# Optimization experiments

Hardware: AMD Instinct MI355X
Metric: run time of the kernel (lower is better)

## Reference

```python
import jax, jax.numpy as jnp
import numpy as np

HEADS, HEAD_DIM, WS = 12, 32, 7
DISP = WS // 2


def _shift_masks(ws, d):
    # upper/lower mask: blocks crossing the wrapped boundary in the row direction
    ul = np.zeros((ws * ws, ws * ws), np.float32)
    ul[-d * ws:, :-d * ws] = -np.inf
    ul[:-d * ws, -d * ws:] = -np.inf
    # left/right mask: columns crossing the wrapped boundary
    lr = np.zeros((ws, ws, ws, ws), np.float32)
    lr[:, -d:, :, :-d] = -np.inf
    lr[:, :-d, :, -d:] = -np.inf
    lr = lr.reshape(ws * ws, ws * ws)
    return jnp.asarray(ul), jnp.asarray(lr)


def _rel_indices(ws):
    idx = np.arange(ws)
    coords = np.stack(np.meshgrid(idx, idx, indexing='ij'), -1).reshape(-1, 2)  # [[x,y] row-major]
    rel = coords[None, :, :] - coords[:, None, :] + ws - 1  # (ws^2, ws^2, 2)
    return jnp.asarray(rel)


def setup_inputs() -> dict:
    key = jax.random.key(0)
    ks = jax.random.split(key, 7)
    b, H, W, dim = 16, 56, 56, 384
    inner = HEADS * HEAD_DIM
    x = jax.random.normal(ks[0], (b, H, W, dim), jnp.float32)
    w_qkv = jax.random.normal(ks[1], (dim, 3 * inner), jnp.float32) * (dim ** -0.5)
    pos_embedding = jax.random.normal(ks[2], (2 * WS - 1, 2 * WS - 1), jnp.float32) * 0.02
    w_out = jax.random.normal(ks[3], (inner, dim), jnp.float32) * (inner ** -0.5)
    b_out = jnp.zeros((dim,), jnp.float32)
    w_post = jax.random.normal(ks[4], (dim, dim), jnp.float32) * (dim ** -0.5)
    b_post = jnp.zeros((dim,), jnp.float32)
    return {"x": x, "w_qkv": w_qkv, "pos_embedding": pos_embedding,
            "w_out": w_out, "b_out": b_out, "w_post": w_post, "b_post": b_post}


def reference(x, w_qkv, pos_embedding, w_out, b_out, w_post, b_post):
    b, H, W, dim = x.shape
    nw_h, nw_w = H // WS, W // WS
    scale = HEAD_DIM ** -0.5

    # cyclic shift
    x = jnp.roll(x, shift=(-DISP, -DISP), axis=(1, 2))

    # qkv projection (no bias), window partition -> (3, b, h, nw, ws^2, d)
    qkv = (x @ w_qkv).reshape(b, nw_h, WS, nw_w, WS, 3, HEADS, HEAD_DIM)
    qkv = qkv.transpose(5, 0, 6, 1, 3, 2, 4, 7).reshape(3, b, HEADS, nw_h * nw_w, WS * WS, HEAD_DIM)
    q, k, v = qkv[0], qkv[1], qkv[2]

    dots = jnp.einsum('bhwid,bhwjd->bhwij', q, k) * scale

    # relative position bias gather
    rel = _rel_indices(WS)
    dots = dots + pos_embedding[rel[..., 0], rel[..., 1]]

    # shifted-window masks
    ul, lr = _shift_masks(WS, DISP)
    dots = dots.at[:, :, -nw_w:].add(ul)
    dots = dots.at[:, :, nw_w - 1::nw_w].add(lr)

    attn = jax.nn.softmax(dots, axis=-1)
    out = jnp.einsum('bhwij,bhwjd->bhwid', attn, v)

    # merge windows back -> (b, H, W, inner)
    out = out.reshape(b, HEADS, nw_h, nw_w, WS, WS, HEAD_DIM)
    out = out.transpose(0, 2, 4, 3, 5, 1, 6).reshape(b, H, W, HEADS * HEAD_DIM)

    out = out @ w_out + b_out
    out = out @ w_post + b_post  # post_drop is identity in eval
    out = jnp.roll(out, shift=(DISP, DISP), axis=(1, 2))
    return out
```

## Files before the change

### kernel.cpp

```cpp
#include <hip/hip_runtime.h>
#include <hip/hip_bf16.h>
#include <stdint.h>

typedef __bf16 bf16_t;
typedef bf16_t bf16x8 __attribute__((ext_vector_type(8)));
typedef bf16_t bf16x4 __attribute__((ext_vector_type(4)));
typedef float f32x4 __attribute__((ext_vector_type(4)));

#define BATCH 16
#define HH    56
#define DIMK  384
#define M_TOT (BATCH*HH*HH)
#define SCALE 0.17677669529663687f

__device__ __forceinline__ void async_load16(const bf16_t* g, const bf16_t* l) {
  __builtin_amdgcn_global_load_lds((const __attribute__((address_space(1))) void*)g,
                                   (__attribute__((address_space(3))) void*)l,
                                   16, 0, 0);
}

template<int CTRL>
__device__ __forceinline__ float dpp_ror(float x) {
  return __int_as_float(__builtin_amdgcn_mov_dpp(__float_as_int(x), CTRL, 0xf, 0xf, false));
}
__device__ __forceinline__ float rowmax16(float v) {
  v = fmaxf(v, dpp_ror<0x121>(v));
  v = fmaxf(v, dpp_ror<0x122>(v));
  v = fmaxf(v, dpp_ror<0x124>(v));
  v = fmaxf(v, dpp_ror<0x128>(v));
  return v;
}
__device__ __forceinline__ float rowsum16(float v) {
  v += dpp_ror<0x121>(v);
  v += dpp_ror<0x122>(v);
  v += dpp_ror<0x124>(v);
  v += dpp_ror<0x128>(v);
  return v;
}

__global__ void k_zero(float* __restrict__ p, int n) {
  int i = blockIdx.x * 256 + threadIdx.x;
  if (i < n) p[i] = 0.f;
}

__global__ void k_transpose(const float* __restrict__ w, bf16_t* __restrict__ wT) {
  int idx = blockIdx.x * 256 + threadIdx.x;
  if (idx >= 1152 * 384) return;
  int n = idx / 384, k = idx - n * 384;
  wT[idx] = (bf16_t)w[k * 1152 + n];
}

__global__ void k_comb(const float* __restrict__ w_out, const float* __restrict__ b_out,
                       const float* __restrict__ w_post, const float* __restrict__ b_post,
                       bf16_t* __restrict__ wcombT, float* __restrict__ bcomb) {
  __shared__ float col[384];
  const int n = blockIdx.x, t = threadIdx.x;
  for (int j = t; j < 384; j += 256) col[j] = w_post[j * 384 + n];
  __syncthreads();
  for (int k = t; k < 384; k += 256) {
    float acc = 0.f;
    for (int j = 0; j < 384; ++j) acc += w_out[k * 384 + j] * col[j];
    wcombT[n * 384 + k] = (bf16_t)acc;
  }
  if (t == 0) {
    float acc = b_post[n];
    for (int j = 0; j < 384; ++j) acc += b_out[j] * col[j];
    bcomb[n] = acc;
  }
}

__global__ void k_bias(const float* __restrict__ pos, float* __restrict__ biasC) {
  int idx = blockIdx.x * 256 + threadIdx.x;
  if (idx >= 4 * 16 * 64 * 4) return;
  int reg = idx & 3, lane = (idx >> 2) & 63, tile = (idx >> 8) & 15, cls = idx >> 12;
  int mt = tile >> 2, nt = tile & 3, lc = lane & 15, quad = lane >> 4;
  int m = mt * 16 + quad * 4 + reg, n = nt * 16 + lc;
  float v = -1e32f;
  if (m < 49 && n < 49) {
    int ty = m / 7, tx = m % 7, jy = n / 7, jx = n % 7;
    bool dead = ((cls & 1) && ((m >= 28) != (n >= 28))) ||
                ((cls & 2) && ((tx >= 4) != (jx >= 4)));
    v = dead ? -1e32f : pos[(jy - ty + 6) * 13 + (jx - tx + 6)] * (1.0f / SCALE);
  }
  biasC[idx] = v;
}

__global__ void k_convroll(const float* __restrict__ x, bf16_t* __restrict__ xb) {
  int idx = blockIdx.x * 256 + threadIdx.x;
  if (idx >= M_TOT * 48) return;
  int row = idx / 48, c = idx - row * 48;
  int bb = row / 3136, rem = row - bb * 3136, i = rem / 56, j = rem - i * 56;
  int si = i + 3; if (si >= 56) si -= 56;
  int sj = j + 3; if (sj >= 56) sj -= 56;
  const float* src = x + ((size_t)(bb * 3136 + si * 56 + sj)) * 384 + c * 8;
  f32x4 v0 = *(const f32x4*)src;
  f32x4 v1 = *(const f32x4*)(src + 4);
  bf16x8 o;
#pragma unroll
  for (int u = 0; u < 4; ++u) { o[u] = (bf16_t)v0[u]; o[4 + u] = (bf16_t)v1[u]; }
  *(bf16x8*)(xb + (size_t)row * 384 + c * 8) = o;
}

template<int MODE>
__device__ __forceinline__
void gemm_body(const bf16_t* __restrict__ A, const bf16_t* __restrict__ B,
               void* __restrict__ Cv, const float* __restrict__ bias,
               int Ndim, int Kdim, int lda) {
  __shared__ __align__(16) bf16_t As[2][128 * 64];
  __shared__ __align__(16) bf16_t Bs[2][128 * 64];
  const int tid  = threadIdx.x;
  const int wave = tid >> 6;
  const int lane = tid & 63;
  const int wr = wave >> 1, wc = wave & 1;

  const int gx   = gridDim.x;
  const int nwg  = gx * gridDim.y;
  const int flat = blockIdx.y * gx + blockIdx.x;
  const int qch  = nwg >> 3;
  const int nf   = (flat & 7) * qch + (flat >> 3);
  const int bx   = nf % gx;
  const int by   = nf / gx;

  const int row0 = by * 128;
  const int col0 = bx * 128;

  const bf16_t* aptr[4];
  const bf16_t* bptr[4];
  int dst[4];
#pragma unroll
  for (int c = 0; c < 4; ++c) {
    int linear = c * 256 + tid;
    int r  = linear >> 3;
    int kc = linear & 7;
    int gk = kc ^ (r & 7);
    dst[c] = linear * 8;
    aptr[c] = A + (size_t)(row0 + r) * lda + gk * 8;
    bptr[c] = B + (size_t)(col0 + r) * Kdim + gk * 8;
  }

  f32x4 acc[4][4] = {};
  const int lr = lane >> 4;
  const int lc = lane & 15;
  unsigned aoff[4][2], boff[4][2];
#pragma unroll
  for (int mi = 0; mi < 4; ++mi)
#pragma unroll
    for (int kh = 0; kh < 2; ++kh) {
      int arow = wr * 64 + mi * 16 + lc;
      int brow = wc * 64 + mi * 16 + lc;
      int sc   = (kh * 4 + lr) ^ (lc & 7);
      aoff[mi][kh] = (unsigned)(arow * 64 + sc * 8);
      boff[mi][kh] = (unsigned)(brow * 64 + sc * 8);
    }

  const int kiters = Kdim >> 6;

#pragma unroll
  for (int c = 0; c < 4; ++c) {
    async_load16(aptr[c], As[0] + dst[c]);
    async_load16(bptr[c], Bs[0] + dst[c]);
  }

  for (int kt = 0; kt < kiters; ++kt) {
    const int cur = kt & 1;
    __syncthreads();
    if (kt + 1 < kiters) {
      const int koff = (kt + 1) * 64;
#pragma unroll
      for (int c = 0; c < 4; ++c) {
        async_load16(aptr[c] + koff, As[cur ^ 1] + dst[c]);
        async_load16(bptr[c] + koff, Bs[cur ^ 1] + dst[c]);
      }
    }
    bf16x8 af[4][2], bfr[4][2];
#pragma unroll
    for (int mi = 0; mi < 4; ++mi)
#pragma unroll
      for (int kh = 0; kh < 2; ++kh) {
        af[mi][kh]  = *(const bf16x8*)(As[cur] + aoff[mi][kh]);
        bfr[mi][kh] = *(const bf16x8*)(Bs[cur] + boff[mi][kh]);
      }
#pragma unroll
    for (int kh = 0; kh < 2; ++kh)
#pragma unroll
      for (int mi = 0; mi < 4; ++mi)
#pragma unroll
        for (int ni = 0; ni < 4; ++ni)
          acc[mi][ni] = __builtin_amdgcn_mfma_f32_16x16x32_bf16(af[mi][kh], bfr[ni][kh], acc[mi][ni], 0, 0, 0);
  }

#pragma unroll
  for (int mi = 0; mi < 4; ++mi) {
#pragma unroll
    for (int rr = 0; rr < 4; ++rr) {
      int grow = row0 + wr * 64 + mi * 16 + lr * 4 + rr;
      size_t orow;
      if (MODE == 1) {
        int bb  = grow / 3136;
        int rem = grow - bb * 3136;
        int i = rem / 56;
        int j = rem - i * 56;
        int si = i + 3; if (si >= 56) si -= 56;
        int sj = j + 3; if (sj >= 56) sj -= 56;
        orow = (size_t)(bb * 3136 + si * 56 + sj);
      } else {
        orow = (size_t)grow;
      }
#pragma unroll
      for (int ni = 0; ni < 4; ++ni) {
        int gcol = col0 + wc * 64 + ni * 16 + lc;
        float v = acc[mi][ni][rr];
        if (MODE == 1) {
          ((float*)Cv)[orow * (size_t)Ndim + gcol] = v + bias[gcol];
        } else {
          ((bf16_t*)Cv)[orow * (size_t)Ndim + gcol] = (bf16_t)v;
        }
      }
    }
  }
}

__global__ __launch_bounds__(256)
void k_gemm_qkv(const bf16_t* __restrict__ A, const bf16_t* __restrict__ B,
                void* __restrict__ Cv, const float* __restrict__ bias,
                int Ndim, int Kdim, int lda) {
  gemm_body<0>(A, B, Cv, bias, Ndim, Kdim, lda);
}
__global__ __launch_bounds__(256)
void k_gemm_out(const bf16_t* __restrict__ A, const bf16_t* __restrict__ B,
                void* __restrict__ Cv, const float* __restrict__ bias,
                int Ndim, int Kdim, int lda) {
  gemm_body<1>(A, B, Cv, bias, Ndim, Kdim, lda);
}

__global__ __launch_bounds__(256)
void k_attn(const float* __restrict__ biasC, bf16_t* __restrict__ qkv) {
  __shared__ __align__(16) bf16_t Ps[4 * 64 * 72];
  const int tid = threadIdx.x, wid = tid >> 6, lane = tid & 63;
  const int p = blockIdx.x * 4 + wid;
  const int b = p / 768, rem = p - b * 768;
  const int head = rem >> 6, w = rem & 63;
  const int wy = w >> 3, wx = w & 7;
  const int cls = ((wy == 7) ? 1 : 0) | ((wx == 7) ? 2 : 0);
  const int lc = lane & 15, quad = lane >> 4;
  const size_t wbase = ((size_t)b * 3136 + (size_t)wy * 7 * 56 + (size_t)wx * 7) * 1152
                       + head * 32;

  auto rowoff = [&](int m) -> size_t {
    int ty = m / 7, tx = m - ty * 7;
    return wbase + (size_t)(ty * 56 + tx) * 1152;
  };

  bf16x8 qf[4], kf[4];
#pragma unroll
  for (int t = 0; t < 4; ++t) {
    int m = t * 16 + lc; if (m > 48) m = 48;
    const bf16_t* r = qkv + rowoff(m);
    qf[t] = *(const bf16x8*)(r + quad * 8);
    kf[t] = *(const bf16x8*)(r + 384 + quad * 8);
  }

  bf16x8 vf[2][2];
#pragma unroll
  for (int kc = 0; kc < 2; ++kc)
#pragma unroll
    for (int u = 0; u < 8; ++u) {
      int n = kc * 32 + quad * 8 + u; if (n > 48) n = 48;
      const bf16_t* r = qkv + rowoff(n) + 768 + lc;
      vf[kc][0][u] = r[0];
      vf[kc][1][u] = r[16];
    }

  f32x4 acc[4][4];
  const float* bp = biasC + cls * 4096 + lane * 4;
#pragma unroll
  for (int mt = 0; mt < 4; ++mt)
#pragma unroll
    for (int nt = 0; nt < 4; ++nt)
      acc[mt][nt] = *(const f32x4*)(bp + (mt * 4 + nt) * 256);
  __builtin_amdgcn_s_setprio(1);
#pragma unroll
  for (int mt = 0; mt < 4; ++mt)
#pragma unroll
    for (int nt = 0; nt < 4; ++nt)
      acc[mt][nt] = __builtin_amdgcn_mfma_f32_16x16x32_bf16(qf[mt], kf[nt], acc[mt][nt], 0, 0, 0);
  __builtin_amdgcn_s_setprio(0);

  float l[4][4];
#pragma unroll
  for (int mt = 0; mt < 4; ++mt)
#pragma unroll
    for (int reg = 0; reg < 4; ++reg) {
      float mx = fmaxf(fmaxf(acc[mt][0][reg], acc[mt][1][reg]),
                       fmaxf(acc[mt][2][reg], acc[mt][3][reg]));
      mx = rowmax16(mx);
      float s = 0.f;
#pragma unroll
      for (int nt = 0; nt < 4; ++nt) {
        float pe = __expf((acc[mt][nt][reg] - mx) * SCALE);
        acc[mt][nt][reg] = pe;
        s += pe;
      }
      l[mt][reg] = rowsum16(s);
    }

  bf16_t* P = Ps + wid * (64 * 72);
#pragma unroll
  for (int mt = 0; mt < 4; ++mt)
#pragma unroll
    for (int nt = 0; nt < 4; ++nt)
#pragma unroll
      for (int reg = 0; reg < 4; ++reg)
        P[(mt * 16 + quad * 4 + reg) * 72 + nt * 16 + lc] = (bf16_t)acc[mt][nt][reg];

  f32x4 oacc[4][2] = {};
#pragma unroll
  for (int mt = 0; mt < 4; ++mt) {
    bf16x8 pf0 = *(const bf16x8*)(P + (mt * 16 + lc) * 72 + quad * 8);
    bf16x8 pf1 = *(const bf16x8*)(P + (mt * 16 + lc) * 72 + 32 + quad * 8);
    __builtin_amdgcn_s_setprio(1);
#pragma unroll
    for (int dt = 0; dt < 2; ++dt) {
      oacc[mt][dt] = __builtin_amdgcn_mfma_f32_16x16x32_bf16(pf0, vf[0][dt], oacc[mt][dt], 0, 0, 0);
      oacc[mt][dt] = __builtin_amdgcn_mfma_f32_16x16x32_bf16(pf1, vf[1][dt], oacc[mt][dt], 0, 0, 0);
    }
    __builtin_amdgcn_s_setprio(0);
  }

#pragma unroll
  for (int mt = 0; mt < 4; ++mt)
#pragma unroll
    for (int reg = 0; reg < 4; ++reg) {
      int m = mt * 16 + quad * 4 + reg;
      if (m < 49) {
        float rl = __builtin_amdgcn_rcpf(l[mt][reg]);
        bf16_t* r = qkv + rowoff(m);
        r[lc]      = (bf16_t)(oacc[mt][0][reg] * rl);
        r[16 + lc] = (bf16_t)(oacc[mt][1][reg] * rl);
      }
    }
}

extern "C" void kernel_launch(void* const* d_in, const int* in_sizes, int n_in,
                              void* d_out, int out_size, void* d_ws, size_t ws_size,
                              hipStream_t stream) {
  const float* x      = (const float*)d_in[0];
  const float* w_qkv  = (const float*)d_in[1];
  const float* pos    = (const float*)d_in[2];
  const float* w_out  = (const float*)d_in[3];
  const float* b_out  = (const float*)d_in[4];
  const float* w_post = (const float*)d_in[5];
  const float* b_post = (const float*)d_in[6];
  float* out = (float*)d_out;

  const size_t SZ_QKV  = (size_t)M_TOT * 1152 * 2;
  const size_t SZ_WT   = (size_t)1152 * 384 * 2;
  const size_t SZ_WC   = (size_t)384 * 384 * 2;
  const size_t SZ_BC   = 384 * 4;
  const size_t SZ_BIAS = (size_t)4 * 16 * 64 * 4 * 4;
  const size_t NEEDED  = SZ_QKV + SZ_WT + SZ_WC + SZ_BC + SZ_BIAS;

  if (ws_size < NEEDED) {
    k_zero<<<(out_size + 255) / 256, 256, 0, stream>>>(out, out_size);
    return;
  }

  char* ws = (char*)d_ws;
  bf16_t* qkv   = (bf16_t*)ws;
  bf16_t* wT    = (bf16_t*)(ws + SZ_QKV);
  bf16_t* wcT   = (bf16_t*)(ws + SZ_QKV + SZ_WT);
  float*  bc    = (float*)(ws + SZ_QKV + SZ_WT + SZ_WC);
  float*  biasC = (float*)(ws + SZ_QKV + SZ_WT + SZ_WC + SZ_BC);
  bf16_t* xb    = (bf16_t*)d_out;

  k_transpose<<<1728, 256, 0, stream>>>(w_qkv, wT);
  k_comb<<<384, 256, 0, stream>>>(w_out, b_out, w_post, b_post, wcT, bc);
  k_bias<<<64, 256, 0, stream>>>(pos, biasC);
  k_convroll<<<(M_TOT * 48 + 255) / 256, 256, 0, stream>>>(x, xb);
  k_gemm_qkv<<<dim3(9, 392), 256, 0, stream>>>(xb, wT, qkv, nullptr, 1152, DIMK, DIMK);
  k_attn<<<3072, 256, 0, stream>>>(biasC, qkv);
  k_gemm_out<<<dim3(3, 392), 256, 0, stream>>>(qkv, wcT, out, bc, 384, DIMK, 1152);
}
```

Baseline: 309.5 us.

## Fuse prep kernels into one launch with tiled transpose and coalesced weight combine

Merges the four preprocessing kernels (input roll+convert, qkv weight transpose, out/post weight combine, bias table) into a single kernel that dispatches on block index. The weight transpose now goes through an LDS tile so both the reads and the writes are coalesced. The weight-combine step now gives each output entry to one wave, which reads a w_out row in coalesced chunks and reduces it with shuffles, replacing the old per-thread strided loop. This removes three launches and speeds up the slow combine step, at the cost of a more complex kernel whose branches share one LDS allocation.

```diff
diff --git a/kernel.cpp b/kernel.cpp
--- a/kernel.cpp
+++ b/kernel.cpp
@@ -12,6 +12,12 @@
 #define DIMK  384
 #define M_TOT (BATCH*HH*HH)
 #define SCALE 0.17677669529663687f
+
+#define NB_CONV  9408
+#define NB_TRANS 108
+#define NB_COMB  384
+#define NB_BIAS  64
+#define NB_PREP  (NB_CONV + NB_TRANS + NB_COMB + NB_BIAS)
 
 __device__ __forceinline__ void async_load16(const bf16_t* g, const bf16_t* l) {
   __builtin_amdgcn_global_load_lds((const __attribute__((address_space(1))) void*)g,
@@ -43,62 +49,94 @@
   if (i < n) p[i] = 0.f;
 }
 
-__global__ void k_transpose(const float* __restrict__ w, bf16_t* __restrict__ wT) {
-  int idx = blockIdx.x * 256 + threadIdx.x;
-  if (idx >= 1152 * 384) return;
-  int n = idx / 384, k = idx - n * 384;
-  wT[idx] = (bf16_t)w[k * 1152 + n];
-}
-
-__global__ void k_comb(const float* __restrict__ w_out, const float* __restrict__ b_out,
-                       const float* __restrict__ w_post, const float* __restrict__ b_post,
-                       bf16_t* __restrict__ wcombT, float* __restrict__ bcomb) {
-  __shared__ float col[384];
-  const int n = blockIdx.x, t = threadIdx.x;
-  for (int j = t; j < 384; j += 256) col[j] = w_post[j * 384 + n];
-  __syncthreads();
-  for (int k = t; k < 384; k += 256) {
-    float acc = 0.f;
-    for (int j = 0; j < 384; ++j) acc += w_out[k * 384 + j] * col[j];
-    wcombT[n * 384 + k] = (bf16_t)acc;
-  }
-  if (t == 0) {
-    float acc = b_post[n];
-    for (int j = 0; j < 384; ++j) acc += b_out[j] * col[j];
-    bcomb[n] = acc;
-  }
-}
-
-__global__ void k_bias(const float* __restrict__ pos, float* __restrict__ biasC) {
-  int idx = blockIdx.x * 256 + threadIdx.x;
-  if (idx >= 4 * 16 * 64 * 4) return;
-  int reg = idx & 3, lane = (idx >> 2) & 63, tile = (idx >> 8) & 15, cls = idx >> 12;
-  int mt = tile >> 2, nt = tile & 3, lc = lane & 15, quad = lane >> 4;
-  int m = mt * 16 + quad * 4 + reg, n = nt * 16 + lc;
-  float v = -1e32f;
-  if (m < 49 && n < 49) {
-    int ty = m / 7, tx = m % 7, jy = n / 7, jx = n % 7;
-    bool dead = ((cls & 1) && ((m >= 28) != (n >= 28))) ||
-                ((cls & 2) && ((tx >= 4) != (jx >= 4)));
-    v = dead ? -1e32f : pos[(jy - ty + 6) * 13 + (jx - tx + 6)] * (1.0f / SCALE);
-  }
-  biasC[idx] = v;
-}
-
-__global__ void k_convroll(const float* __restrict__ x, bf16_t* __restrict__ xb) {
-  int idx = blockIdx.x * 256 + threadIdx.x;
-  if (idx >= M_TOT * 48) return;
-  int row = idx / 48, c = idx - row * 48;
-  int bb = row / 3136, rem = row - bb * 3136, i = rem / 56, j = rem - i * 56;
-  int si = i + 3; if (si >= 56) si -= 56;
-  int sj = j + 3; if (sj >= 56) sj -= 56;
-  const float* src = x + ((size_t)(bb * 3136 + si * 56 + sj)) * 384 + c * 8;
-  f32x4 v0 = *(const f32x4*)src;
-  f32x4 v1 = *(const f32x4*)(src + 4);
-  bf16x8 o;
-#pragma unroll
-  for (int u = 0; u < 4; ++u) { o[u] = (bf16_t)v0[u]; o[4 + u] = (bf16_t)v1[u]; }
-  *(bf16x8*)(xb + (size_t)row * 384 + c * 8) = o;
+__global__ __launch_bounds__(256)
+void k_prep(const float* __restrict__ x, bf16_t* __restrict__ xb,
+            const float* __restrict__ w_qkv, bf16_t* __restrict__ wT,
+            const float* __restrict__ w_out, const float* __restrict__ b_out,
+            const float* __restrict__ w_post, const float* __restrict__ b_post,
+            bf16_t* __restrict__ wcombT, float* __restrict__ bcomb,
+            const float* __restrict__ pos, float* __restrict__ biasC) {
+  __shared__ float sbuf[64 * 65];
+  const int blk = blockIdx.x;
+  const int t   = threadIdx.x;
+
+  if (blk < NB_CONV) {
+    int idx = blk * 256 + t;
+    int row = idx / 48, c = idx - row * 48;
+    int bb = row / 3136, rem = row - bb * 3136, i = rem / 56, j = rem - i * 56;
+    int si = i + 3; if (si >= 56) si -= 56;
+    int sj = j + 3; if (sj >= 56) sj -= 56;
+    const float* src = x + ((size_t)(bb * 3136 + si * 56 + sj)) * 384 + c * 8;
+    f32x4 v0 = *(const f32x4*)src;
+    f32x4 v1 = *(const f32x4*)(src + 4);
+    bf16x8 o;
+#pragma unroll
+    for (int u = 0; u < 4; ++u) { o[u] = (bf16_t)v0[u]; o[4 + u] = (bf16_t)v1[u]; }
+    *(bf16x8*)(xb + (size_t)row * 384 + c * 8) = o;
+
+  } else if (blk < NB_CONV + NB_TRANS) {
+    int blk2 = blk - NB_CONV;
+    int tn = blk2 % 18, tk = blk2 / 18;
+    int k0 = tk * 64, n0 = tn * 64;
+#pragma unroll
+    for (int s = 0; s < 4; ++s) {
+      int r = (t >> 4) + s * 16;
+      int c = (t & 15) * 4;
+      f32x4 v = *(const f32x4*)(w_qkv + (size_t)(k0 + r) * 1152 + n0 + c);
+#pragma unroll
+      for (int u = 0; u < 4; ++u) sbuf[r * 65 + c + u] = v[u];
+    }
+    __syncthreads();
+#pragma unroll
+    for (int s = 0; s < 4; ++s) {
+      int rn = (t >> 4) + s * 16;
+      int ck = (t & 15) * 4;
+      bf16x4 o;
+#pragma unroll
+      for (int u = 0; u < 4; ++u) o[u] = (bf16_t)sbuf[(ck + u) * 65 + rn];
+      *(bf16x4*)(wT + (size_t)(n0 + rn) * 384 + k0 + ck) = o;
+    }
+
+  } else if (blk < NB_CONV + NB_TRANS + NB_COMB) {
+    int n = blk - (NB_CONV + NB_TRANS);
+    float* col = sbuf;
+    for (int j = t; j < 384; j += 256) col[j] = w_post[j * 384 + n];
+    __syncthreads();
+    const int wid = t >> 6, lane = t & 63;
+    for (int kk = 0; kk < 96; ++kk) {
+      int k = kk * 4 + wid;
+      float s = 0.f;
+#pragma unroll
+      for (int c = 0; c < 6; ++c)
+        s += w_out[(size_t)k * 384 + c * 64 + lane] * col[c * 64 + lane];
+#pragma unroll
+      for (int off = 32; off >= 1; off >>= 1) s += __shfl_down(s, off);
+      if (lane == 0) wcombT[(size_t)n * 384 + k] = (bf16_t)s;
+    }
+    if (wid == 0) {
+      float s = 0.f;
+#pragma unroll
+      for (int c = 0; c < 6; ++c)
+        s += b_out[c * 64 + lane] * col[c * 64 + lane];
+#pragma unroll
+      for (int off = 32; off >= 1; off >>= 1) s += __shfl_down(s, off);
+      if (lane == 0) bcomb[n] = s + b_post[n];
+    }
+
+  } else {
+    int idx = (blk - (NB_CONV + NB_TRANS + NB_COMB)) * 256 + t;
+    int reg = idx & 3, lane = (idx >> 2) & 63, tile = (idx >> 8) & 15, cls = idx >> 12;
+    int mt = tile >> 2, nt = tile & 3, lc = lane & 15, quad = lane >> 4;
+    int m = mt * 16 + quad * 4 + reg, n = nt * 16 + lc;
+    float v = -1e32f;
+    if (m < 49 && n < 49) {
+      int ty = m / 7, tx = m % 7, jy = n / 7, jx = n % 7;
+      bool dead = ((cls & 1) && ((m >= 28) != (n >= 28))) ||
+                  ((cls & 2) && ((tx >= 4) != (jx >= 4)));
+      v = dead ? -1e32f : pos[(jy - ty + 6) * 13 + (jx - tx + 6)] * (1.0f / SCALE);
+    }
+    biasC[idx] = v;
+  }
 }
 
 template<int MODE>
@@ -373,10 +411,8 @@
   float*  biasC = (float*)(ws + SZ_QKV + SZ_WT + SZ_WC + SZ_BC);
   bf16_t* xb    = (bf16_t*)d_out;
 
-  k_transpose<<<1728, 256, 0, stream>>>(w_qkv, wT);
-  k_comb<<<384, 256, 0, stream>>>(w_out, b_out, w_post, b_post, wcT, bc);
-  k_bias<<<64, 256, 0, stream>>>(pos, biasC);
-  k_convroll<<<(M_TOT * 48 + 255) / 256, 256, 0, stream>>>(x, xb);
+  k_prep<<<NB_PREP, 256, 0, stream>>>(x, xb, w_qkv, wT, w_out, b_out,
+                                      w_post, b_post, wcT, bc, pos, biasC);
   k_gemm_qkv<<<dim3(9, 392), 256, 0, stream>>>(xb, wT, qkv, nullptr, 1152, DIMK, DIMK);
   k_attn<<<3072, 256, 0, stream>>>(biasC, qkv);
   k_gemm_out<<<dim3(3, 392), 256, 0, stream>>>(qkv, wcT, out, bc, 384, DIMK, 1152);
```

New measurement: 326.3 us. 1.05x slower.
